# Optimization experiments

Hardware: AMD Instinct MI355X
Metric: run time of the kernel (lower is better)

## Reference

```python
import jax, jax.numpy as jnp
import numpy as np

D_MODEL = 1024
N_HEADS = 16
HEAD_DIM = D_MODEL // N_HEADS
FFN_HIDDEN = 4096
EPS = 1e-6


def setup_inputs() -> dict:
    key = jax.random.key(0)
    ks = jax.random.split(key, 12)
    B, L, D, F = 4, 2048, D_MODEL, FFN_HIDDEN
    s = 0.02
    return {
        "x": jax.random.normal(ks[0], (B, L, D), jnp.float32),
        "rel_pos_bias": jax.random.normal(ks[1], (1, N_HEADS, L, L), jnp.float32) * 0.1,
        "wq": jax.random.normal(ks[2], (D, D), jnp.float32) * s,
        "bq": jnp.zeros((D,), jnp.float32),
        "wk": jax.random.normal(ks[3], (D, D), jnp.float32) * s,
        "bk": jnp.zeros((D,), jnp.float32),
        "wv": jax.random.normal(ks[4], (D, D), jnp.float32) * s,
        "bv": jnp.zeros((D,), jnp.float32),
        "wo": jax.random.normal(ks[5], (D, D), jnp.float32) * s,
        "bo": jnp.zeros((D,), jnp.float32),
        "norm1_w": jnp.ones((D,), jnp.float32),
        "norm2_w": jnp.ones((D,), jnp.float32),
        "w1": jax.random.normal(ks[6], (F, D), jnp.float32) * s,
        "b1": jnp.zeros((F,), jnp.float32),
        "w2": jax.random.normal(ks[7], (D, F), jnp.float32) * s,
        "b2": jnp.zeros((D,), jnp.float32),
    }


def _rmsnorm(x, w):
    rms = jnp.sqrt(jnp.mean(x * x, axis=-1, keepdims=True) + EPS)
    return x / rms * w


def reference(x, rel_pos_bias, wq, bq, wk, bk, wv, bv, wo, bo, norm1_w, norm2_w, w1, b1, w2, b2):
    B, L, D = x.shape
    H, hd = N_HEADS, HEAD_DIM
    scale = hd ** -0.5

    # ---- attention (pre-norm) ----
    h = _rmsnorm(x, norm1_w)
    q = (h @ wq.T + bq).reshape(B, L, H, hd).transpose(0, 2, 1, 3)  # [B,H,L,hd]
    k = (h @ wk.T + bk).reshape(B, L, H, hd).transpose(0, 2, 1, 3)
    v = (h @ wv.T + bv).reshape(B, L, H, hd).transpose(0, 2, 1, 3)

    scores = jnp.einsum("bhqd,bhkd->bhqk", q, k) * scale  # [B,H,L,L]
    causal = jnp.tril(jnp.ones((L, L), bool))
    scores = jnp.where(causal, scores, -jnp.inf)
    scores = scores + rel_pos_bias  # additive bias after masking, as in torch
    attn = jax.nn.softmax(scores, axis=-1)

    out = jnp.einsum("bhqk,bhkd->bhqd", attn, v)  # [B,H,L,hd]
    out = out.transpose(0, 2, 1, 3).reshape(B, L, D)
    out = out @ wo.T + bo
    x = x + out

    # ---- FFN (pre-norm): Linear -> SiLU -> Linear ----
    h = _rmsnorm(x, norm2_w)
    f = jax.nn.silu(h @ w1.T + b1) @ w2.T + b2
    return x + f
```

## Files before the change

kernel.cpp:

```cpp
#include <hip/hip_runtime.h>

typedef unsigned short u16;
#define MB ((size_t)1 << 20)

typedef __attribute__((ext_vector_type(8))) short short8;
typedef __attribute__((ext_vector_type(4))) float float4v;

__device__ __forceinline__ float bfu(u16 s) { return __uint_as_float(((unsigned)s) << 16); }
__device__ __forceinline__ u16 f2bf(float f) {
  unsigned u = __float_as_uint(f);
  return (u16)((u + 0x7fffu + ((u >> 16) & 1u)) >> 16);
}
__device__ __forceinline__ void async_ld16(const u16* g, u16* l) {
  __builtin_amdgcn_global_load_lds((const __attribute__((address_space(1))) unsigned*)g,
                                   (__attribute__((address_space(3))) unsigned*)l, 16, 0, 0);
}

__global__ __launch_bounds__(256)
void cvt_k(const float* __restrict__ in, u16* __restrict__ out, int n4) {
  int i = blockIdx.x * 256 + threadIdx.x;
  if (i >= n4) return;
  float4 v = ((const float4*)in)[i];
  ushort4 p;
  p.x = f2bf(v.x); p.y = f2bf(v.y); p.z = f2bf(v.z); p.w = f2bf(v.w);
  ((ushort4*)out)[i] = p;
}

__global__ __launch_bounds__(256)
void rmsnorm_k(const float* __restrict__ x, const float* __restrict__ g,
               u16* __restrict__ o) {
  int row = blockIdx.x;
  int t = threadIdx.x;
  float4 v = ((const float4*)(x + (size_t)row * 1024))[t];
  float ss = v.x * v.x + v.y * v.y + v.z * v.z + v.w * v.w;
#pragma unroll
  for (int d = 32; d; d >>= 1) ss += __shfl_down(ss, d);
  __shared__ float r[4];
  if ((t & 63) == 0) r[t >> 6] = ss;
  __syncthreads();
  float rinv = rsqrtf((r[0] + r[1] + r[2] + r[3]) * (1.0f / 1024.0f) + 1e-6f);
  float4 gv = ((const float4*)g)[t];
  ushort4 p;
  p.x = f2bf(v.x * rinv * gv.x);
  p.y = f2bf(v.y * rinv * gv.y);
  p.z = f2bf(v.z * rinv * gv.z);
  p.w = f2bf(v.w * rinv * gv.w);
  ((ushort4*)(o + (size_t)row * 1024))[t] = p;
}

__global__ __launch_bounds__(256)
void rmsnorm_bf_k(const u16* __restrict__ x, const float* __restrict__ g,
                  u16* __restrict__ o) {
  int row = blockIdx.x;
  int t = threadIdx.x;
  ushort4 v = ((const ushort4*)(x + (size_t)row * 1024))[t];
  float f0 = bfu(v.x), f1 = bfu(v.y), f2 = bfu(v.z), f3 = bfu(v.w);
  float ss = f0 * f0 + f1 * f1 + f2 * f2 + f3 * f3;
#pragma unroll
  for (int d = 32; d; d >>= 1) ss += __shfl_down(ss, d);
  __shared__ float r[4];
  if ((t & 63) == 0) r[t >> 6] = ss;
  __syncthreads();
  float rinv = rsqrtf((r[0] + r[1] + r[2] + r[3]) * (1.0f / 1024.0f) + 1e-6f);
  float4 gv = ((const float4*)g)[t];
  ushort4 p;
  p.x = f2bf(f0 * rinv * gv.x);
  p.y = f2bf(f1 * rinv * gv.y);
  p.z = f2bf(f2 * rinv * gv.z);
  p.w = f2bf(f3 * rinv * gv.w);
  ((ushort4*)(o + (size_t)row * 1024))[t] = p;
}

template <int EPI>
__global__ __launch_bounds__(256)
void gemm_mfma(const u16* __restrict__ A, const u16* __restrict__ B,
               const float* __restrict__ bias, const void* __restrict__ res,
               void* __restrict__ outp, int M, int N, int K) {
  __shared__ u16 As[128 * 32];
  __shared__ u16 Bs[128 * 32];
  int t = threadIdx.x;
  int m0 = blockIdx.y * 128, n0 = blockIdx.x * 128;
  int w = t >> 6, lane = t & 63;
  int quad = lane >> 4, l16 = lane & 15;
  int wm = w >> 1, wn = w & 1;

  float4v acc[4][4];
#pragma unroll
  for (int mi = 0; mi < 4; mi++)
#pragma unroll
    for (int ni = 0; ni < 4; ni++) acc[mi][ni] = (float4v){0.f, 0.f, 0.f, 0.f};

  const u16* ga = A + (size_t)(m0 + (t >> 2)) * K + (t & 3) * 8;
  const u16* gb = B + (size_t)(n0 + (t >> 2)) * K + (t & 3) * 8;
  u16* la = As + w * 512;
  u16* lb = Bs + w * 512;
  const size_t rstep = (size_t)64 * K;

  for (int k0 = 0; k0 < K; k0 += 32) {
    async_ld16(ga + k0, la);
    async_ld16(ga + rstep + k0, la + 2048);
    async_ld16(gb + k0, lb);
    async_ld16(gb + rstep + k0, lb + 2048);
    __syncthreads();

    short8 af[4], bf[4];
#pragma unroll
    for (int i = 0; i < 4; i++)
      af[i] = *(const short8*)&As[(wm * 64 + i * 16 + l16) * 32 + quad * 8];
#pragma unroll
    for (int i = 0; i < 4; i++)
      bf[i] = *(const short8*)&Bs[(wn * 64 + i * 16 + l16) * 32 + quad * 8];
#pragma unroll
    for (int mi = 0; mi < 4; mi++)
#pragma unroll
      for (int ni = 0; ni < 4; ni++)
        acc[mi][ni] = __builtin_amdgcn_mfma_f32_16x16x32_bf16(af[mi], bf[ni],
                                                              acc[mi][ni], 0, 0, 0);
    __syncthreads();
  }

  int rbase = m0 + wm * 64;
  int cbase = n0 + wn * 64;
  float bv[4];
#pragma unroll
  for (int ni = 0; ni < 4; ni++) bv[ni] = bias[cbase + ni * 16 + l16];
#pragma unroll
  for (int mi = 0; mi < 4; mi++) {
#pragma unroll
    for (int r = 0; r < 4; r++) {
      int row = rbase + mi * 16 + quad * 4 + r;
#pragma unroll
      for (int ni = 0; ni < 4; ni++) {
        int col = cbase + ni * 16 + l16;
        float o = acc[mi][ni][r] + bv[ni];
        if (EPI == 1) o = o / (1.0f + __expf(-o));
        if (EPI == 3) o += ((const float*)res)[(size_t)row * N + col];
        if (EPI == 4) o += bfu(((const u16*)res)[(size_t)row * N + col]);
        if (EPI == 4)
          ((float*)outp)[(size_t)row * N + col] = o;
        else
          ((u16*)outp)[(size_t)row * N + col] = f2bf(o);
      }
    }
  }
}

#define QKVS 3072
__global__ __launch_bounds__(256)
void attn_mfma_k(const u16* __restrict__ QKV, const float* __restrict__ bias,
                 u16* __restrict__ O) {
  const int L = 2048, Dm = 1024;
  __shared__ u16 Ks[64 * 64];
  __shared__ u16 QP[64][72];
  __shared__ u16 Vts[64][72];

  int t = threadIdx.x;
  int qt = blockIdx.x;
  int bh = blockIdx.y;
  int h = bh >> 2, b = bh & 3;
  int qbase = qt * 64;
  size_t base = ((size_t)b * L) * QKVS + (size_t)h * 64;
  const u16* Qp = QKV + base;
  const u16* Kp = QKV + base + 1024;
  const u16* Vp = QKV + base + 2048;
  size_t obase = ((size_t)b * L) * Dm + (size_t)h * 64;
  const float* brow = bias + (size_t)h * L * L;

  int w = t >> 6, lane = t & 63, quad = lane >> 4, l16 = lane & 15;

  {
    int row = t >> 2, d0 = (t & 3) * 16;
    const u16* src = Qp + (size_t)(qbase + row) * QKVS + d0;
    uint4 v0 = *(const uint4*)src;
    uint4 v1 = *(const uint4*)(src + 8);
    *(uint4*)&QP[row][d0] = v0;
    *(uint4*)&QP[row][d0 + 8] = v1;
  }
  __syncthreads();

  short8 qf0 = *(const short8*)&QP[w * 16 + l16][quad * 8];
  short8 qf1 = *(const short8*)&QP[w * 16 + l16][32 + quad * 8];

  float4v acc[4];
#pragma unroll
  for (int d4 = 0; d4 < 4; d4++) acc[d4] = (float4v){0.f, 0.f, 0.f, 0.f};
  float sloc[4] = {0.f, 0.f, 0.f, 0.f};
  int rbase = qbase + w * 16 + quad * 4;

  int krow = t >> 3;
  int kcc = ((t & 7) ^ (krow & 7)) * 8;
  const u16* gk = Kp + (size_t)krow * QKVS + kcc;
  u16* lk = Ks + w * 512;
  const size_t kstep = (size_t)32 * QKVS;

  int ntiles = qt + 1;
  for (int it = 0; it < ntiles; it++) {
    int j0 = it * 64;

    float bv[4][4];
#pragma unroll
    for (int t4 = 0; t4 < 4; t4++) {
      int kidx = j0 + t4 * 16 + l16;
#pragma unroll
      for (int r = 0; r < 4; r++)
        bv[t4][r] = brow[(size_t)(rbase + r) * L + kidx];
    }

    async_ld16(gk + (size_t)j0 * QKVS, lk);
    async_ld16(gk + (size_t)j0 * QKVS + kstep, lk + 2048);

    {
      int kp = t >> 3, d0 = (t & 7) * 8;
      const u16* s0 = Vp + (size_t)(j0 + 2 * kp) * QKVS + d0;
      union { uint4 v; u16 e[8]; } ua, ub;
      ua.v = *(const uint4*)s0;
      ub.v = *(const uint4*)(s0 + QKVS);
#pragma unroll
      for (int i = 0; i < 8; i++)
        *(unsigned*)&Vts[d0 + i][2 * kp] =
            (unsigned)ua.e[i] | ((unsigned)ub.e[i] << 16);
    }
    __syncthreads();

    float4v s[4];
#pragma unroll
    for (int t4 = 0; t4 < 4; t4++) {
      int key = t4 * 16 + l16;
      const u16* kr = Ks + key * 64;
      int p0 = ((quad ^ (key & 7)) * 8);
      short8 kf0 = *(const short8*)(kr + p0);
      short8 kf1 = *(const short8*)(kr + (p0 ^ 32));
      float4v z = (float4v){0.f, 0.f, 0.f, 0.f};
      z = __builtin_amdgcn_mfma_f32_16x16x32_bf16(qf0, kf0, z, 0, 0, 0);
      z = __builtin_amdgcn_mfma_f32_16x16x32_bf16(qf1, kf1, z, 0, 0, 0);
      s[t4] = z;
    }

#pragma unroll
    for (int t4 = 0; t4 < 4; t4++) {
      int kidx = j0 + t4 * 16 + l16;
#pragma unroll
      for (int r = 0; r < 4; r++) {
        float p = (kidx > rbase + r)
                      ? 0.f
                      : __expf(fmaf(s[t4][r], 0.125f, bv[t4][r]));
        sloc[r] += p;
        QP[w * 16 + quad * 4 + r][t4 * 16 + l16] = f2bf(p);
      }
    }

#pragma unroll
    for (int c = 0; c < 2; c++) {
      short8 pf = *(const short8*)&QP[w * 16 + l16][c * 32 + quad * 8];
#pragma unroll
      for (int d4 = 0; d4 < 4; d4++) {
        short8 vf = *(const short8*)&Vts[d4 * 16 + l16][c * 32 + quad * 8];
        acc[d4] = __builtin_amdgcn_mfma_f32_16x16x32_bf16(pf, vf, acc[d4], 0, 0, 0);
      }
    }
    __syncthreads();
  }

#pragma unroll
  for (int r = 0; r < 4; r++) {
    float sum = sloc[r];
    sum += __shfl_xor(sum, 1);
    sum += __shfl_xor(sum, 2);
    sum += __shfl_xor(sum, 4);
    sum += __shfl_xor(sum, 8);
    float inv = 1.0f / sum;
    u16* orow = O + obase + (size_t)(rbase + r) * Dm;
#pragma unroll
    for (int d4 = 0; d4 < 4; d4++) orow[d4 * 16 + l16] = f2bf(acc[d4][r] * inv);
  }
}

extern "C" void kernel_launch(void* const* d_in, const int* in_sizes, int n_in,
                              void* d_out, int out_size, void* d_ws, size_t ws_size,
                              hipStream_t stream) {
  const float* x = (const float*)d_in[0];
  const float* rb = (const float*)d_in[1];
  const float* wq = (const float*)d_in[2];
  const float* bq = (const float*)d_in[3];
  const float* wk = (const float*)d_in[4];
  const float* bk = (const float*)d_in[5];
  const float* wv = (const float*)d_in[6];
  const float* bv = (const float*)d_in[7];
  const float* wo = (const float*)d_in[8];
  const float* bo = (const float*)d_in[9];
  const float* n1w = (const float*)d_in[10];
  const float* n2w = (const float*)d_in[11];
  const float* w1 = (const float*)d_in[12];
  const float* b1 = (const float*)d_in[13];
  const float* w2 = (const float*)d_in[14];
  const float* b2 = (const float*)d_in[15];

  const int M = 8192, D = 1024, F = 4096;

  char* wsp = (char*)d_ws;
  u16* h = (u16*)(wsp);
  u16* ao = (u16*)(wsp);
  u16* f1 = (u16*)(wsp);
  u16* qkv = (u16*)(wsp + 16 * MB);
  u16* x1b = (u16*)(wsp + 64 * MB);
  u16* h2 = (u16*)(wsp + 80 * MB);
  float* bqkv = (float*)(wsp + 80 * MB);
  u16* wqkvb = (u16*)(wsp + 96 * MB);
  u16* wob = (u16*)(wsp + 102 * MB);
  u16* w1b = (u16*)(wsp + 104 * MB);
  u16* w2b = (u16*)(wsp + 96 * MB);

  dim3 blk(256);

  cvt_k<<<1024, blk, 0, stream>>>(wq, wqkvb, (D * D) / 4);
  cvt_k<<<1024, blk, 0, stream>>>(wk, wqkvb + D * D, (D * D) / 4);
  cvt_k<<<1024, blk, 0, stream>>>(wv, wqkvb + 2 * D * D, (D * D) / 4);
  cvt_k<<<1024, blk, 0, stream>>>(wo, wob, (D * D) / 4);
  cvt_k<<<4096, blk, 0, stream>>>(w1, w1b, (F * D) / 4);
  hipMemcpyAsync(bqkv, bq, D * 4, hipMemcpyDeviceToDevice, stream);
  hipMemcpyAsync(bqkv + D, bk, D * 4, hipMemcpyDeviceToDevice, stream);
  hipMemcpyAsync(bqkv + 2 * D, bv, D * 4, hipMemcpyDeviceToDevice, stream);

  rmsnorm_k<<<M, blk, 0, stream>>>(x, n1w, h);
  gemm_mfma<0><<<dim3(3 * D / 128, M / 128), blk, 0, stream>>>(
      h, wqkvb, bqkv, nullptr, qkv, M, 3 * D, D);
  attn_mfma_k<<<dim3(32, 64), blk, 0, stream>>>(qkv, rb, ao);
  gemm_mfma<3><<<dim3(D / 128, M / 128), blk, 0, stream>>>(
      ao, wob, bo, x, x1b, M, D, D);
  cvt_k<<<4096, blk, 0, stream>>>(w2, w2b, (D * F) / 4);
  rmsnorm_bf_k<<<M, blk, 0, stream>>>(x1b, n2w, h2);
  gemm_mfma<1><<<dim3(F / 128, M / 128), blk, 0, stream>>>(
      h2, w1b, b1, nullptr, f1, M, F, D);
  gemm_mfma<4><<<dim3(D / 128, M / 128), blk, 0, stream>>>(
      f1, w2b, b2, x1b, d_out, M, D, F);
}
```

Measured before the change: 916.7 us.

## Pair causal query tiles per attention block, double-buffer K/V, swizzle GEMM grid

The attention kernel now gives each block two query tiles (p and 31-p), so every block does the same amount of causal work and K/V tiles are shared between both tiles. K and V are double-buffered, and the next tile's K, V and bias loads are prefetched while the current tile is computed. The V transpose layout in LDS is XOR-swizzled to cut bank conflicts, and launch bounds ask for 3 blocks per CU. The GEMM remaps block IDs in an XCD-aware pattern for better L2 locality. In exchange it uses more registers and LDS per block and launches half as many attention blocks.

```diff
diff --git a/kernel.cpp b/kernel.cpp
--- a/kernel.cpp
+++ b/kernel.cpp
@@ -79,7 +79,12 @@
   __shared__ u16 As[128 * 32];
   __shared__ u16 Bs[128 * 32];
   int t = threadIdx.x;
-  int m0 = blockIdx.y * 128, n0 = blockIdx.x * 128;
+  unsigned gx = gridDim.x;
+  unsigned nwg = gx * gridDim.y;
+  unsigned flat = blockIdx.y * gx + blockIdx.x;
+  unsigned cpx = nwg >> 3;
+  unsigned swz = (flat & 7) * cpx + (flat >> 3);
+  int m0 = (int)(swz / gx) * 128, n0 = (int)(swz % gx) * 128;
   int w = t >> 6, lane = t & 63;
   int quad = lane >> 4, l16 = lane & 15;
   int wm = w >> 1, wn = w & 1;
@@ -146,19 +151,62 @@
 }
 
 #define QKVS 3072
-__global__ __launch_bounds__(256)
+
+__device__ __forceinline__ void attn_phase(
+    const u16* __restrict__ ksb, const u16 (*vts)[72], u16 (*qp)[72],
+    short8 qf0, short8 qf1, const float (&bv)[4][4],
+    int j0, int rX, int w, int quad, int l16,
+    float4v (&acc)[4], float (&sl)[4]) {
+  float4v s[4];
+#pragma unroll
+  for (int t4 = 0; t4 < 4; t4++) {
+    int key = t4 * 16 + l16;
+    const u16* kr = ksb + key * 64;
+    int p0 = (quad ^ (key & 7)) * 8;
+    short8 kf0 = *(const short8*)(kr + p0);
+    short8 kf1 = *(const short8*)(kr + (p0 ^ 32));
+    float4v z = (float4v){0.f, 0.f, 0.f, 0.f};
+    z = __builtin_amdgcn_mfma_f32_16x16x32_bf16(qf0, kf0, z, 0, 0, 0);
+    z = __builtin_amdgcn_mfma_f32_16x16x32_bf16(qf1, kf1, z, 0, 0, 0);
+    s[t4] = z;
+  }
+#pragma unroll
+  for (int t4 = 0; t4 < 4; t4++) {
+    int kidx = j0 + t4 * 16 + l16;
+#pragma unroll
+    for (int r = 0; r < 4; r++) {
+      float pv = (kidx > rX + r) ? 0.f : __expf(fmaf(s[t4][r], 0.125f, bv[t4][r]));
+      sl[r] += pv;
+      qp[w * 16 + quad * 4 + r][t4 * 16 + l16] = f2bf(pv);
+    }
+  }
+#pragma unroll
+  for (int c = 0; c < 2; c++) {
+    short8 pf = *(const short8*)&qp[w * 16 + l16][c * 32 + quad * 8];
+#pragma unroll
+    for (int d4 = 0; d4 < 4; d4++) {
+      int row = d4 * 16 + l16;
+      int ch = ((c * 4 + quad) ^ (2 * d4 + (l16 >> 3))) * 16;
+      short8 vf = *(const short8*)((const char*)&vts[row][0] + ch);
+      acc[d4] = __builtin_amdgcn_mfma_f32_16x16x32_bf16(pf, vf, acc[d4], 0, 0, 0);
+    }
+  }
+}
+
+__global__ __launch_bounds__(256, 3)
 void attn_mfma_k(const u16* __restrict__ QKV, const float* __restrict__ bias,
                  u16* __restrict__ O) {
   const int L = 2048, Dm = 1024;
-  __shared__ u16 Ks[64 * 64];
+  __shared__ u16 Ks[2][64 * 64];
+  __shared__ u16 Vts[2][64][72];
   __shared__ u16 QP[64][72];
-  __shared__ u16 Vts[64][72];
 
   int t = threadIdx.x;
-  int qt = blockIdx.x;
+  int p = blockIdx.x;
+  int qtA = p, qtB = 31 - p;
+  int nj = qtB + 1;
   int bh = blockIdx.y;
   int h = bh >> 2, b = bh & 3;
-  int qbase = qt * 64;
   size_t base = ((size_t)b * L) * QKVS + (size_t)h * 64;
   const u16* Qp = QKV + base;
   const u16* Kp = QKV + base + 1024;
@@ -167,111 +215,140 @@
   const float* brow = bias + (size_t)h * L * L;
 
   int w = t >> 6, lane = t & 63, quad = lane >> 4, l16 = lane & 15;
-
-  {
-    int row = t >> 2, d0 = (t & 3) * 16;
-    const u16* src = Qp + (size_t)(qbase + row) * QKVS + d0;
-    uint4 v0 = *(const uint4*)src;
-    uint4 v1 = *(const uint4*)(src + 8);
-    *(uint4*)&QP[row][d0] = v0;
-    *(uint4*)&QP[row][d0 + 8] = v1;
-  }
-  __syncthreads();
-
-  short8 qf0 = *(const short8*)&QP[w * 16 + l16][quad * 8];
-  short8 qf1 = *(const short8*)&QP[w * 16 + l16][32 + quad * 8];
-
-  float4v acc[4];
-#pragma unroll
-  for (int d4 = 0; d4 < 4; d4++) acc[d4] = (float4v){0.f, 0.f, 0.f, 0.f};
-  float sloc[4] = {0.f, 0.f, 0.f, 0.f};
-  int rbase = qbase + w * 16 + quad * 4;
+  int rA = qtA * 64 + w * 16 + quad * 4;
+  int rB = qtB * 64 + w * 16 + quad * 4;
+
+  int qrow = t >> 2, qd0 = (t & 3) * 16;
+  const u16* qsA = Qp + (size_t)(qtA * 64 + qrow) * QKVS + qd0;
+  const u16* qsB = Qp + (size_t)(qtB * 64 + qrow) * QKVS + qd0;
+  uint4 qa0 = *(const uint4*)qsA;
+  uint4 qa1 = *(const uint4*)(qsA + 8);
+  uint4 qb0 = *(const uint4*)qsB;
+  uint4 qb1 = *(const uint4*)(qsB + 8);
+
+  int vkp = t >> 3, vd0 = (t & 7) * 8;
+  const u16* vsrc = Vp + (size_t)(2 * vkp) * QKVS + vd0;
+  union U8 { uint4 v; u16 e[8]; };
+  U8 va, vb;
+  va.v = *(const uint4*)vsrc;
+  vb.v = *(const uint4*)(vsrc + QKVS);
 
   int krow = t >> 3;
   int kcc = ((t & 7) ^ (krow & 7)) * 8;
   const u16* gk = Kp + (size_t)krow * QKVS + kcc;
-  u16* lk = Ks + w * 512;
-  const size_t kstep = (size_t)32 * QKVS;
-
-  int ntiles = qt + 1;
-  for (int it = 0; it < ntiles; it++) {
-    int j0 = it * 64;
-
-    float bv[4][4];
-#pragma unroll
-    for (int t4 = 0; t4 < 4; t4++) {
-      int kidx = j0 + t4 * 16 + l16;
-#pragma unroll
-      for (int r = 0; r < 4; r++)
-        bv[t4][r] = brow[(size_t)(rbase + r) * L + kidx];
-    }
-
-    async_ld16(gk + (size_t)j0 * QKVS, lk);
-    async_ld16(gk + (size_t)j0 * QKVS + kstep, lk + 2048);
-
-    {
-      int kp = t >> 3, d0 = (t & 7) * 8;
-      const u16* s0 = Vp + (size_t)(j0 + 2 * kp) * QKVS + d0;
-      union { uint4 v; u16 e[8]; } ua, ub;
-      ua.v = *(const uint4*)s0;
-      ub.v = *(const uint4*)(s0 + QKVS);
-#pragma unroll
-      for (int i = 0; i < 8; i++)
-        *(unsigned*)&Vts[d0 + i][2 * kp] =
-            (unsigned)ua.e[i] | ((unsigned)ub.e[i] << 16);
+  async_ld16(gk, Ks[0] + w * 512);
+  async_ld16(gk + (size_t)32 * QKVS, Ks[0] + w * 512 + 2048);
+
+  float bvA[4][4], bvB[4][4];
+#pragma unroll
+  for (int t4 = 0; t4 < 4; t4++)
+#pragma unroll
+    for (int r = 0; r < 4; r++) {
+      bvA[t4][r] = brow[(size_t)(rA + r) * L + t4 * 16 + l16];
+      bvB[t4][r] = brow[(size_t)(rB + r) * L + t4 * 16 + l16];
+    }
+
+  *(uint4*)&QP[qrow][qd0] = qa0;
+  *(uint4*)&QP[qrow][qd0 + 8] = qa1;
+  *(uint4*)&Vts[1][qrow][qd0] = qb0;
+  *(uint4*)&Vts[1][qrow][qd0 + 8] = qb1;
+#pragma unroll
+  for (int i = 0; i < 8; i++) {
+    int row = vd0 + i;
+    int ch = ((vkp >> 2) ^ (t & 7)) * 16 + (vkp & 3) * 4;
+    *(unsigned*)((char*)&Vts[0][row][0] + ch) =
+        (unsigned)va.e[i] | ((unsigned)vb.e[i] << 16);
+  }
+  __syncthreads();
+
+  short8 qfA0 = *(const short8*)&QP[w * 16 + l16][quad * 8];
+  short8 qfA1 = *(const short8*)&QP[w * 16 + l16][32 + quad * 8];
+  short8 qfB0 = *(const short8*)&Vts[1][w * 16 + l16][quad * 8];
+  short8 qfB1 = *(const short8*)&Vts[1][w * 16 + l16][32 + quad * 8];
+  __syncthreads();
+
+  float4v accA[4], accB[4];
+  float slA[4] = {0.f, 0.f, 0.f, 0.f}, slB[4] = {0.f, 0.f, 0.f, 0.f};
+#pragma unroll
+  for (int d4 = 0; d4 < 4; d4++) {
+    accA[d4] = (float4v){0.f, 0.f, 0.f, 0.f};
+    accB[d4] = (float4v){0.f, 0.f, 0.f, 0.f};
+  }
+
+  for (int j = 0; j < nj; j++) {
+    int buf = j & 1, nb = buf ^ 1;
+    int j0 = j * 64;
+    int stage = (j + 1 < nj);
+    int phA = (j <= qtA);
+    int phAn = (j + 1 <= qtA);
+    float bvAn[4][4], bvBn[4][4];
+
+    if (stage) {
+      va.v = *(const uint4*)(vsrc + (size_t)(j0 + 64) * QKVS);
+      vb.v = *(const uint4*)(vsrc + (size_t)(j0 + 64) * QKVS + QKVS);
+      async_ld16(gk + (size_t)(j0 + 64) * QKVS, Ks[nb] + w * 512);
+      async_ld16(gk + (size_t)(j0 + 96) * QKVS, Ks[nb] + w * 512 + 2048);
+#pragma unroll
+      for (int t4 = 0; t4 < 4; t4++)
+#pragma unroll
+        for (int r = 0; r < 4; r++)
+          bvBn[t4][r] = brow[(size_t)(rB + r) * L + j0 + 64 + t4 * 16 + l16];
+    }
+
+    if (phA)
+      attn_phase(Ks[buf], Vts[buf], QP, qfA0, qfA1, bvA, j0, rA, w, quad, l16, accA, slA);
+
+    if (stage) {
+#pragma unroll
+      for (int i = 0; i < 8; i++) {
+        int row = vd0 + i;
+        int ch = ((vkp >> 2) ^ (t & 7)) * 16 + (vkp & 3) * 4;
+        *(unsigned*)((char*)&Vts[nb][row][0] + ch) =
+            (unsigned)va.e[i] | ((unsigned)vb.e[i] << 16);
+      }
+      if (phAn) {
+#pragma unroll
+        for (int t4 = 0; t4 < 4; t4++)
+#pragma unroll
+          for (int r = 0; r < 4; r++)
+            bvAn[t4][r] = brow[(size_t)(rA + r) * L + j0 + 64 + t4 * 16 + l16];
+      }
+    }
+
+    attn_phase(Ks[buf], Vts[buf], QP, qfB0, qfB1, bvB, j0, rB, w, quad, l16, accB, slB);
+
+    if (stage) {
+#pragma unroll
+      for (int t4 = 0; t4 < 4; t4++)
+#pragma unroll
+        for (int r = 0; r < 4; r++) bvB[t4][r] = bvBn[t4][r];
+    }
+    if (phAn) {
+#pragma unroll
+      for (int t4 = 0; t4 < 4; t4++)
+#pragma unroll
+        for (int r = 0; r < 4; r++) bvA[t4][r] = bvAn[t4][r];
     }
     __syncthreads();
-
-    float4v s[4];
-#pragma unroll
-    for (int t4 = 0; t4 < 4; t4++) {
-      int key = t4 * 16 + l16;
-      const u16* kr = Ks + key * 64;
-      int p0 = ((quad ^ (key & 7)) * 8);
-      short8 kf0 = *(const short8*)(kr + p0);
-      short8 kf1 = *(const short8*)(kr + (p0 ^ 32));
-      float4v z = (float4v){0.f, 0.f, 0.f, 0.f};
-      z = __builtin_amdgcn_mfma_f32_16x16x32_bf16(qf0, kf0, z, 0, 0, 0);
-      z = __builtin_amdgcn_mfma_f32_16x16x32_bf16(qf1, kf1, z, 0, 0, 0);
-      s[t4] = z;
-    }
-
-#pragma unroll
-    for (int t4 = 0; t4 < 4; t4++) {
-      int kidx = j0 + t4 * 16 + l16;
-#pragma unroll
-      for (int r = 0; r < 4; r++) {
-        float p = (kidx > rbase + r)
-                      ? 0.f
-                      : __expf(fmaf(s[t4][r], 0.125f, bv[t4][r]));
-        sloc[r] += p;
-        QP[w * 16 + quad * 4 + r][t4 * 16 + l16] = f2bf(p);
-      }
-    }
-
-#pragma unroll
-    for (int c = 0; c < 2; c++) {
-      short8 pf = *(const short8*)&QP[w * 16 + l16][c * 32 + quad * 8];
-#pragma unroll
-      for (int d4 = 0; d4 < 4; d4++) {
-        short8 vf = *(const short8*)&Vts[d4 * 16 + l16][c * 32 + quad * 8];
-        acc[d4] = __builtin_amdgcn_mfma_f32_16x16x32_bf16(pf, vf, acc[d4], 0, 0, 0);
-      }
-    }
-    __syncthreads();
   }
 
 #pragma unroll
   for (int r = 0; r < 4; r++) {
-    float sum = sloc[r];
-    sum += __shfl_xor(sum, 1);
-    sum += __shfl_xor(sum, 2);
-    sum += __shfl_xor(sum, 4);
-    sum += __shfl_xor(sum, 8);
-    float inv = 1.0f / sum;
-    u16* orow = O + obase + (size_t)(rbase + r) * Dm;
-#pragma unroll
-    for (int d4 = 0; d4 < 4; d4++) orow[d4 * 16 + l16] = f2bf(acc[d4][r] * inv);
+    float sa = slA[r];
+    sa += __shfl_xor(sa, 1); sa += __shfl_xor(sa, 2);
+    sa += __shfl_xor(sa, 4); sa += __shfl_xor(sa, 8);
+    float ia = 1.0f / sa;
+    u16* oa = O + obase + (size_t)(rA + r) * Dm;
+#pragma unroll
+    for (int d4 = 0; d4 < 4; d4++) oa[d4 * 16 + l16] = f2bf(accA[d4][r] * ia);
+
+    float sb = slB[r];
+    sb += __shfl_xor(sb, 1); sb += __shfl_xor(sb, 2);
+    sb += __shfl_xor(sb, 4); sb += __shfl_xor(sb, 8);
+    float ib = 1.0f / sb;
+    u16* ob = O + obase + (size_t)(rB + r) * Dm;
+#pragma unroll
+    for (int d4 = 0; d4 < 4; d4++) ob[d4 * 16 + l16] = f2bf(accB[d4][r] * ib);
   }
 }
 
@@ -324,7 +401,7 @@
   rmsnorm_k<<<M, blk, 0, stream>>>(x, n1w, h);
   gemm_mfma<0><<<dim3(3 * D / 128, M / 128), blk, 0, stream>>>(
       h, wqkvb, bqkv, nullptr, qkv, M, 3 * D, D);
-  attn_mfma_k<<<dim3(32, 64), blk, 0, stream>>>(qkv, rb, ao);
+  attn_mfma_k<<<dim3(16, 64), blk, 0, stream>>>(qkv, rb, ao);
   gemm_mfma<3><<<dim3(D / 128, M / 128), blk, 0, stream>>>(
       ao, wob, bo, x, x1b, M, D, D);
   cvt_k<<<4096, blk, 0, stream>>>(w2, w2b, (D * F) / 4);
```

Result: slower. 1.053 ms (+14.9%).

## Pair query tiles per 512-thread attention block with double-buffered K/V prefetch

Applied to the files above, without the earlier changes.

The attention kernel now runs 512 threads per block covering two adjacent query tiles, so each K/V tile is loaded once and shared by both. K and V are double-buffered, with the next tile's K (async to LDS), V and bias fetched while the current tile is computed. The transposed V layout in LDS is XOR-swizzled to cut bank conflicts, and s_setprio is raised around the MFMA sections. Blocks are issued heaviest-first to balance the causal workload, and the GEMM kernel gains an XCD-aware block index swizzle. The cost is more LDS per block and fewer, larger blocks, which may lower occupancy.

```diff
diff --git a/kernel.cpp b/kernel.cpp
--- a/kernel.cpp
+++ b/kernel.cpp
@@ -79,7 +79,12 @@
   __shared__ u16 As[128 * 32];
   __shared__ u16 Bs[128 * 32];
   int t = threadIdx.x;
-  int m0 = blockIdx.y * 128, n0 = blockIdx.x * 128;
+  unsigned gx = gridDim.x;
+  unsigned nwg = gx * gridDim.y;
+  unsigned flat = blockIdx.y * gx + blockIdx.x;
+  unsigned cpx = nwg >> 3;
+  unsigned swz = (flat & 7) * cpx + (flat >> 3);
+  int m0 = (int)(swz / gx) * 128, n0 = (int)(swz % gx) * 128;
   int w = t >> 6, lane = t & 63;
   int quad = lane >> 4, l16 = lane & 15;
   int wm = w >> 1, wn = w & 1;
@@ -146,19 +151,21 @@
 }
 
 #define QKVS 3072
-__global__ __launch_bounds__(256)
+
+__global__ __launch_bounds__(512, 4)
 void attn_mfma_k(const u16* __restrict__ QKV, const float* __restrict__ bias,
                  u16* __restrict__ O) {
   const int L = 2048, Dm = 1024;
-  __shared__ u16 Ks[64 * 64];
-  __shared__ u16 QP[64][72];
-  __shared__ u16 Vts[64][72];
+  __shared__ u16 Ks[2][64 * 64];
+  __shared__ u16 Vts[2][64][72];
+  __shared__ u16 QP[128][72];
 
   int t = threadIdx.x;
-  int qt = blockIdx.x;
+  int pp = 15 - (int)blockIdx.x;
+  int qtA = 2 * pp, qtB = 2 * pp + 1;
+  int nj = qtB + 1;
   int bh = blockIdx.y;
   int h = bh >> 2, b = bh & 3;
-  int qbase = qt * 64;
   size_t base = ((size_t)b * L) * QKVS + (size_t)h * 64;
   const u16* Qp = QKV + base;
   const u16* Kp = QKV + base + 1024;
@@ -167,67 +174,73 @@
   const float* brow = bias + (size_t)h * L * L;
 
   int w = t >> 6, lane = t & 63, quad = lane >> 4, l16 = lane & 15;
-
-  {
-    int row = t >> 2, d0 = (t & 3) * 16;
-    const u16* src = Qp + (size_t)(qbase + row) * QKVS + d0;
-    uint4 v0 = *(const uint4*)src;
-    uint4 v1 = *(const uint4*)(src + 8);
-    *(uint4*)&QP[row][d0] = v0;
-    *(uint4*)&QP[row][d0 + 8] = v1;
-  }
-  __syncthreads();
-
-  short8 qf0 = *(const short8*)&QP[w * 16 + l16][quad * 8];
-  short8 qf1 = *(const short8*)&QP[w * 16 + l16][32 + quad * 8];
-
-  float4v acc[4];
-#pragma unroll
-  for (int d4 = 0; d4 < 4; d4++) acc[d4] = (float4v){0.f, 0.f, 0.f, 0.f};
-  float sloc[4] = {0.f, 0.f, 0.f, 0.f};
-  int rbase = qbase + w * 16 + quad * 4;
+  int myqt = (w < 4) ? qtA : qtB;
+  int rX = myqt * 64 + (w & 3) * 16 + quad * 4;
+
+  int qrow = t >> 2, qd0 = (t & 3) * 16;
+  int qglob = (qrow < 64) ? (qtA * 64 + qrow) : (qtB * 64 + (qrow & 63));
+  const u16* qs = Qp + (size_t)qglob * QKVS + qd0;
+  uint4 q0 = *(const uint4*)qs;
+  uint4 q1 = *(const uint4*)(qs + 8);
+
+  int vkp = (t & 255) >> 3;
+  int vd0 = (t & 7) * 8;
+  int vhalf = (t >> 8) * 4;
+  const u16* vsrc = Vp + (size_t)(2 * vkp) * QKVS + vd0;
+  union U8 { uint4 v; u16 e[8]; };
+  U8 va, vb;
+  va.v = *(const uint4*)vsrc;
+  vb.v = *(const uint4*)(vsrc + QKVS);
 
   int krow = t >> 3;
   int kcc = ((t & 7) ^ (krow & 7)) * 8;
   const u16* gk = Kp + (size_t)krow * QKVS + kcc;
-  u16* lk = Ks + w * 512;
-  const size_t kstep = (size_t)32 * QKVS;
-
-  int ntiles = qt + 1;
-  for (int it = 0; it < ntiles; it++) {
-    int j0 = it * 64;
-
-    float bv[4][4];
-#pragma unroll
-    for (int t4 = 0; t4 < 4; t4++) {
-      int kidx = j0 + t4 * 16 + l16;
-#pragma unroll
-      for (int r = 0; r < 4; r++)
-        bv[t4][r] = brow[(size_t)(rbase + r) * L + kidx];
-    }
-
-    async_ld16(gk + (size_t)j0 * QKVS, lk);
-    async_ld16(gk + (size_t)j0 * QKVS + kstep, lk + 2048);
-
-    {
-      int kp = t >> 3, d0 = (t & 7) * 8;
-      const u16* s0 = Vp + (size_t)(j0 + 2 * kp) * QKVS + d0;
-      union { uint4 v; u16 e[8]; } ua, ub;
-      ua.v = *(const uint4*)s0;
-      ub.v = *(const uint4*)(s0 + QKVS);
-#pragma unroll
-      for (int i = 0; i < 8; i++)
-        *(unsigned*)&Vts[d0 + i][2 * kp] =
-            (unsigned)ua.e[i] | ((unsigned)ub.e[i] << 16);
-    }
-    __syncthreads();
-
+  async_ld16(gk, Ks[0] + w * 512);
+
+  float bv[4][4];
+#pragma unroll
+  for (int t4 = 0; t4 < 4; t4++)
+#pragma unroll
+    for (int r = 0; r < 4; r++)
+      bv[t4][r] = brow[(size_t)(rX + r) * L + t4 * 16 + l16];
+
+  *(uint4*)&QP[qrow][qd0] = q0;
+  *(uint4*)&QP[qrow][qd0 + 8] = q1;
+#pragma unroll
+  for (int ii = 0; ii < 4; ii++) {
+    int i = vhalf + ii;
+    int row = vd0 + i;
+    int ch = ((vkp >> 2) ^ (t & 7)) * 16 + (vkp & 3) * 4;
+    *(unsigned*)((char*)&Vts[0][row][0] + ch) =
+        (unsigned)va.e[i] | ((unsigned)vb.e[i] << 16);
+  }
+  __syncthreads();
+
+  short8 qf0 = *(const short8*)&QP[w * 16 + l16][quad * 8];
+  short8 qf1 = *(const short8*)&QP[w * 16 + l16][32 + quad * 8];
+
+  float4v acc[4];
+  float sl[4] = {0.f, 0.f, 0.f, 0.f};
+#pragma unroll
+  for (int d4 = 0; d4 < 4; d4++) acc[d4] = (float4v){0.f, 0.f, 0.f, 0.f};
+
+  for (int j = 0; j < nj; j++) {
+    int buf = j & 1, nb = buf ^ 1;
+    int j0 = j * 64;
+    int stage = (j + 1 < nj);
+    int jn = stage ? j0 + 64 : 0;
+
+    va.v = *(const uint4*)(vsrc + (size_t)jn * QKVS);
+    vb.v = *(const uint4*)(vsrc + (size_t)jn * QKVS + QKVS);
+    if (stage) async_ld16(gk + (size_t)jn * QKVS, Ks[nb] + w * 512);
+
+    __builtin_amdgcn_s_setprio(1);
     float4v s[4];
 #pragma unroll
     for (int t4 = 0; t4 < 4; t4++) {
       int key = t4 * 16 + l16;
-      const u16* kr = Ks + key * 64;
-      int p0 = ((quad ^ (key & 7)) * 8);
+      const u16* kr = Ks[buf] + key * 64;
+      int p0 = (quad ^ (key & 7)) * 8;
       short8 kf0 = *(const short8*)(kr + p0);
       short8 kf1 = *(const short8*)(kr + (p0 ^ 32));
       float4v z = (float4v){0.f, 0.f, 0.f, 0.f};
@@ -235,43 +248,61 @@
       z = __builtin_amdgcn_mfma_f32_16x16x32_bf16(qf1, kf1, z, 0, 0, 0);
       s[t4] = z;
     }
+    __builtin_amdgcn_s_setprio(0);
 
 #pragma unroll
     for (int t4 = 0; t4 < 4; t4++) {
       int kidx = j0 + t4 * 16 + l16;
 #pragma unroll
       for (int r = 0; r < 4; r++) {
-        float p = (kidx > rbase + r)
-                      ? 0.f
-                      : __expf(fmaf(s[t4][r], 0.125f, bv[t4][r]));
-        sloc[r] += p;
-        QP[w * 16 + quad * 4 + r][t4 * 16 + l16] = f2bf(p);
+        float pv = (kidx > rX + r) ? 0.f
+                                   : __expf(fmaf(s[t4][r], 0.125f, bv[t4][r]));
+        sl[r] += pv;
+        QP[w * 16 + quad * 4 + r][t4 * 16 + l16] = f2bf(pv);
       }
     }
 
+#pragma unroll
+    for (int t4 = 0; t4 < 4; t4++)
+#pragma unroll
+      for (int r = 0; r < 4; r++)
+        bv[t4][r] = brow[(size_t)(rX + r) * L + jn + t4 * 16 + l16];
+
+    __builtin_amdgcn_s_setprio(1);
 #pragma unroll
     for (int c = 0; c < 2; c++) {
       short8 pf = *(const short8*)&QP[w * 16 + l16][c * 32 + quad * 8];
 #pragma unroll
       for (int d4 = 0; d4 < 4; d4++) {
-        short8 vf = *(const short8*)&Vts[d4 * 16 + l16][c * 32 + quad * 8];
+        int row = d4 * 16 + l16;
+        int ch = ((c * 4 + quad) ^ (2 * d4 + (l16 >> 3))) * 16;
+        short8 vf = *(const short8*)((const char*)&Vts[buf][row][0] + ch);
         acc[d4] = __builtin_amdgcn_mfma_f32_16x16x32_bf16(pf, vf, acc[d4], 0, 0, 0);
       }
     }
+    __builtin_amdgcn_s_setprio(0);
+
+#pragma unroll
+    for (int ii = 0; ii < 4; ii++) {
+      int i = vhalf + ii;
+      int row = vd0 + i;
+      int ch = ((vkp >> 2) ^ (t & 7)) * 16 + (vkp & 3) * 4;
+      *(unsigned*)((char*)&Vts[nb][row][0] + ch) =
+          (unsigned)va.e[i] | ((unsigned)vb.e[i] << 16);
+    }
+
     __syncthreads();
   }
 
 #pragma unroll
   for (int r = 0; r < 4; r++) {
-    float sum = sloc[r];
-    sum += __shfl_xor(sum, 1);
-    sum += __shfl_xor(sum, 2);
-    sum += __shfl_xor(sum, 4);
-    sum += __shfl_xor(sum, 8);
-    float inv = 1.0f / sum;
-    u16* orow = O + obase + (size_t)(rbase + r) * Dm;
-#pragma unroll
-    for (int d4 = 0; d4 < 4; d4++) orow[d4 * 16 + l16] = f2bf(acc[d4][r] * inv);
+    float sa = sl[r];
+    sa += __shfl_xor(sa, 1); sa += __shfl_xor(sa, 2);
+    sa += __shfl_xor(sa, 4); sa += __shfl_xor(sa, 8);
+    float ia = 1.0f / sa;
+    u16* orow = O + obase + (size_t)(rX + r) * Dm;
+#pragma unroll
+    for (int d4 = 0; d4 < 4; d4++) orow[d4 * 16 + l16] = f2bf(acc[d4][r] * ia);
   }
 }
 
@@ -324,7 +355,7 @@
   rmsnorm_k<<<M, blk, 0, stream>>>(x, n1w, h);
   gemm_mfma<0><<<dim3(3 * D / 128, M / 128), blk, 0, stream>>>(
       h, wqkvb, bqkv, nullptr, qkv, M, 3 * D, D);
-  attn_mfma_k<<<dim3(32, 64), blk, 0, stream>>>(qkv, rb, ao);
+  attn_mfma_k<<<dim3(16, 64), dim3(512), 0, stream>>>(qkv, rb, ao);
   gemm_mfma<3><<<dim3(D / 128, M / 128), blk, 0, stream>>>(
       ao, wob, bo, x, x1b, M, D, D);
   cvt_k<<<4096, blk, 0, stream>>>(w2, w2b, (D * F) / 4);
```

After: 950.0 us. +3.6%, slower.
